# Optimization experiments

Hardware: AMD Instinct MI355X
Metric: run time of the kernel (lower is better)

The kernel has to match this reference:

```python
import jax, jax.numpy as jnp
import numpy as np

B, CQ, CKV, H, W = 8, 256, 512, 64, 64
HKV, WKV = 32, 32
DQK = CQ // 8  # 32


def setup_inputs() -> dict:
    key = jax.random.key(0)
    ks = jax.random.split(key, 9)
    s = 0.05
    return {
        "query": jax.random.normal(ks[0], (B, CQ, H, W), jnp.float32),
        "key_value": jax.random.normal(ks[1], (B, CKV, HKV, WKV), jnp.float32),
        "Wq": jax.random.normal(ks[2], (DQK, CQ), jnp.float32) * s,
        "bq": jax.random.normal(ks[3], (DQK,), jnp.float32) * s,
        "Wk": jax.random.normal(ks[4], (DQK, CKV), jnp.float32) * s,
        "bk": jax.random.normal(ks[5], (DQK,), jnp.float32) * s,
        "Wv": jax.random.normal(ks[6], (CQ, CKV), jnp.float32) * s,
        "bv": jax.random.normal(ks[7], (CQ,), jnp.float32) * s,
        "gamma": jax.random.normal(ks[8], (1,), jnp.float32) * 0.5,
    }


def reference(query, key_value, Wq, bq, Wk, bk, Wv, bv, gamma):
    b, cq, h, w = query.shape
    n = h * w
    # bilinear resize of key_value to query's spatial size (align_corners=False
    # half-pixel convention, matching torch F.interpolate and jax.image.resize)
    kv = jax.image.resize(key_value, (b, key_value.shape[1], h, w), method="bilinear")
    # 1x1 convs are channel contractions
    q = jnp.einsum("bchw,dc->bdhw", query, Wq) + bq[None, :, None, None]   # [B,DQK,H,W]
    k = jnp.einsum("bchw,dc->bdhw", kv, Wk) + bk[None, :, None, None]      # [B,DQK,H,W]
    v = jnp.einsum("bchw,dc->bdhw", kv, Wv) + bv[None, :, None, None]      # [B,CQ,H,W]
    qf = q.reshape(b, -1, n)   # [B,DQK,N]
    kf = k.reshape(b, -1, n)   # [B,DQK,N]
    vf = v.reshape(b, -1, n)   # [B,CQ,N]
    energy = jnp.einsum("bdn,bdm->bnm", qf, kf)        # [B,N,N]
    attention = jax.nn.softmax(energy, axis=-1)
    out = jnp.einsum("bnm,bcm->bcn", attention, vf)     # [B,CQ,N]
    out = out.reshape(b, cq, h, w)
    return gamma[0] * out + query
```

## Files before the change

### kernel.cpp

```cpp
#include <hip/hip_runtime.h>

#define B_ 8
#define CQ_ 256
#define CKV_ 512
#define N_ 4096
#define DQK_ 32

typedef __bf16 bf16;
typedef __bf16 bf16x4 __attribute__((ext_vector_type(4)));
typedef __bf16 bf16x8 __attribute__((ext_vector_type(8)));
typedef float f32x4 __attribute__((ext_vector_type(4)));

__global__ void k_convert_w(const float* __restrict__ Wq, const float* __restrict__ Wk,
                            const float* __restrict__ Wv,
                            bf16* __restrict__ wq, bf16* __restrict__ wk, bf16* __restrict__ wv) {
    int i = blockIdx.x * 256 + threadIdx.x;
    if (i < 8192) wq[i] = (bf16)Wq[i];
    else if (i < 24576) wk[i - 8192] = (bf16)Wk[i - 8192];
    else if (i < 155648) wv[i - 24576] = (bf16)Wv[i - 24576];
}

__global__ __launch_bounds__(256) void k_resize(const float* __restrict__ kv, bf16* __restrict__ kvr) {
    const int yo = blockIdx.x;
    const int b  = blockIdx.y;
    const int tid = threadIdx.x;
    __shared__ float r0[64][33];
    __shared__ float r1[64][33];
    int ty = yo >> 1;
    int y0, y1; float wy0, wy1;
    if ((yo & 1) == 0) { y0 = ty > 0 ? ty - 1 : 0; y1 = ty; wy0 = 0.25f; wy1 = 0.75f; }
    else               { y0 = ty; y1 = ty < 31 ? ty + 1 : 31; wy0 = 0.75f; wy1 = 0.25f; }
    const int u_loc = tid & 63;
    const int xo_base = tid >> 6;
    for (int uc = 0; uc < CKV_; uc += 64) {
        __syncthreads();
        for (int i = 0; i < 8; ++i) {
            int idx = tid + i * 256;
            int u = idx >> 5, x = idx & 31;
            const float* src = kv + ((size_t)b * CKV_ + uc + u) * 1024 + x;
            r0[u][x] = src[y0 * 32];
            r1[u][x] = src[y1 * 32];
        }
        __syncthreads();
        for (int i = 0; i < 16; ++i) {
            int xo = xo_base + i * 4;
            int tx = xo >> 1;
            int xa, xb; float wxa, wxb;
            if ((xo & 1) == 0) { xa = tx > 0 ? tx - 1 : 0; xb = tx; wxa = 0.25f; wxb = 0.75f; }
            else               { xa = tx; xb = tx < 31 ? tx + 1 : 31; wxa = 0.75f; wxb = 0.25f; }
            float v0 = wxa * r0[u_loc][xa] + wxb * r0[u_loc][xb];
            float v1 = wxa * r1[u_loc][xa] + wxb * r1[u_loc][xb];
            float val = wy0 * v0 + wy1 * v1;
            kvr[((size_t)b * N_ + yo * 64 + xo) * CKV_ + uc + u_loc] = (bf16)val;
        }
    }
}

__global__ __launch_bounds__(256) void k_proj_q_fused(const float* __restrict__ query,
                                                      const bf16* __restrict__ W,
                                                      const float* __restrict__ bias,
                                                      bf16* __restrict__ qTb) {
    __shared__ bf16 tile[64][264];
    const int n0 = blockIdx.x * 64;
    const int b  = blockIdx.y;
    const int tid = threadIdx.x;
    const int xi = tid & 15, c0 = tid >> 4;
    for (int pass = 0; pass < 16; ++pass) {
        int c = c0 + pass * 16;
        const float4 v = *(const float4*)(query + ((size_t)b * CQ_ + c) * N_ + n0 + xi * 4);
        tile[xi * 4 + 0][c] = (bf16)v.x;
        tile[xi * 4 + 1][c] = (bf16)v.y;
        tile[xi * 4 + 2][c] = (bf16)v.z;
        tile[xi * 4 + 3][c] = (bf16)v.w;
    }
    __syncthreads();
    const int w = tid >> 6, lane = tid & 63;
    const int l16 = lane & 15, quad = lane >> 4;
    const int ct = w & 1, nh = w >> 1;
    f32x4 acc[2];
    acc[0] = (f32x4){0.f, 0.f, 0.f, 0.f}; acc[1] = (f32x4){0.f, 0.f, 0.f, 0.f};
    const bf16* aptr = W + (ct * 16 + l16) * CQ_ + quad * 8;
#pragma unroll
    for (int ks = 0; ks < 8; ++ks) {
        bf16x8 af = *(const bf16x8*)(aptr + ks * 32);
        for (int j = 0; j < 2; ++j) {
            bf16x8 bfv = *(const bf16x8*)&tile[nh * 32 + j * 16 + l16][ks * 32 + quad * 8];
            acc[j] = __builtin_amdgcn_mfma_f32_16x16x32_bf16(af, bfv, acc[j], 0, 0, 0);
        }
    }
    const float LOG2E = 1.4426950408889634f;
    for (int j = 0; j < 2; ++j)
        for (int r = 0; r < 4; ++r) {
            int d = ct * 16 + quad * 4 + r;
            int n = n0 + nh * 32 + j * 16 + l16;
            qTb[((size_t)b * N_ + n) * DQK_ + d] = (bf16)((acc[j][r] + bias[d]) * LOG2E);
        }
}

__global__ __launch_bounds__(256) void k_proj_k(const bf16* __restrict__ W,
                                                const float* __restrict__ bias,
                                                const bf16* __restrict__ Bm,
                                                bf16* __restrict__ outT) {
    const int mb = blockIdx.x * 128;
    const int b  = blockIdx.y;
    const int tid = threadIdx.x;
    const int w = tid >> 6, lane = tid & 63;
    const int l16 = lane & 15, quad = lane >> 4;
    const int ct = w & 1;
    const int mhalf = (w >> 1) * 64;
    f32x4 acc[4];
    for (int j = 0; j < 4; ++j) acc[j] = (f32x4){0.f, 0.f, 0.f, 0.f};
    const bf16* aptr  = W + (ct * 16 + l16) * CKV_ + quad * 8;
    const bf16* bbase = Bm + ((size_t)b * N_ + mb + mhalf) * CKV_ + quad * 8;
#pragma unroll
    for (int ks = 0; ks < 16; ++ks) {
        bf16x8 af = *(const bf16x8*)(aptr + ks * 32);
        for (int j = 0; j < 4; ++j) {
            bf16x8 bfv = *(const bf16x8*)(bbase + (size_t)(j * 16 + l16) * CKV_ + ks * 32);
            acc[j] = __builtin_amdgcn_mfma_f32_16x16x32_bf16(af, bfv, acc[j], 0, 0, 0);
        }
    }
    for (int j = 0; j < 4; ++j)
        for (int r = 0; r < 4; ++r) {
            int d = ct * 16 + quad * 4 + r;
            int m = mb + mhalf + j * 16 + l16;
            outT[((size_t)b * N_ + m) * DQK_ + d] = (bf16)(acc[j][r] + bias[d]);
        }
}

__global__ __launch_bounds__(256) void k_proj_v(const bf16* __restrict__ W,
                                                const float* __restrict__ bias,
                                                const bf16* __restrict__ Bm,
                                                bf16* __restrict__ vout) {
    const int mb = blockIdx.x * 64;
    const int b  = blockIdx.y;
    const int tid = threadIdx.x;
    const int w = tid >> 6, lane = tid & 63;
    const int l16 = lane & 15, quad = lane >> 4;
    f32x4 acc[4][4];
    for (int i = 0; i < 4; ++i) for (int j = 0; j < 4; ++j) acc[i][j] = (f32x4){0.f, 0.f, 0.f, 0.f};
    const bf16* bbase = Bm + ((size_t)b * N_ + mb) * CKV_ + quad * 8;
#pragma unroll 4
    for (int ks = 0; ks < 16; ++ks) {
        bf16x8 bfv[4];
        for (int j = 0; j < 4; ++j)
            bfv[j] = *(const bf16x8*)(bbase + (size_t)(j * 16 + l16) * CKV_ + ks * 32);
        for (int i = 0; i < 4; ++i) {
            bf16x8 af = *(const bf16x8*)(W + (size_t)((w * 4 + i) * 16 + l16) * CKV_ + ks * 32 + quad * 8);
            for (int j = 0; j < 4; ++j)
                acc[i][j] = __builtin_amdgcn_mfma_f32_16x16x32_bf16(af, bfv[j], acc[i][j], 0, 0, 0);
        }
    }
    for (int i = 0; i < 4; ++i)
        for (int r = 0; r < 4; ++r) {
            int c = (w * 4 + i) * 16 + quad * 4 + r;
            float bvs = bias[c];
            for (int j = 0; j < 4; ++j) {
                int m = mb + j * 16 + l16;
                vout[((size_t)b * CQ_ + c) * N_ + m] = (bf16)(acc[i][j][r] + bvs);
            }
        }
}

__global__ __launch_bounds__(256, 2) void k_flash(const bf16* __restrict__ qT,
                                                  const bf16* __restrict__ kT,
                                                  const bf16* __restrict__ vv,
                                                  const float* __restrict__ query,
                                                  const float* __restrict__ gamma,
                                                  float* __restrict__ out) {
    __shared__ bf16 P[2][64][72];
    const int b  = blockIdx.x;
    const int n0 = blockIdx.y * 64;
    const int tid = threadIdx.x;
    const int w = tid >> 6, lane = tid & 63;
    const int l16 = lane & 15, quad = lane >> 4;
    const int swz = (l16 & 3) ^ ((l16 >> 3) << 1);

    bf16x8 qfrag = *(const bf16x8*)(qT + ((size_t)b * N_ + n0 + w * 16 + l16) * DQK_ + quad * 8);

    const bf16 one = (bf16)1.0f;
    const bf16x8 ones = {one, one, one, one, one, one, one, one};
    const f32x4 zed = {0.f, 0.f, 0.f, 0.f};

    f32x4 acc[4][4];
    for (int i = 0; i < 4; ++i) for (int j = 0; j < 4; ++j) acc[i][j] = zed;
    f32x4 accl[4];
    for (int j = 0; j < 4; ++j) accl[j] = zed;

    const bf16* kbase = kT + (size_t)b * N_ * DQK_;
    const bf16* vbase = vv + ((size_t)b * CQ_ + w * 64) * N_;

    for (int im = 0; im < 4; ++im) {
        bf16x8 kf = *(const bf16x8*)(kbase + (size_t)(im * 16 + l16) * DQK_ + quad * 8);
        f32x4 s = __builtin_amdgcn_mfma_f32_16x16x32_bf16(kf, qfrag, zed, 0, 0, 0);
        bf16x4 pk;
        for (int r = 0; r < 4; ++r) pk[r] = (bf16)__builtin_amdgcn_exp2f(s[r]);
        *(bf16x4*)&P[0][w * 16 + l16][((im ^ swz) << 4) + quad * 4] = pk;
    }

    for (int mt = 0; mt < 64; ++mt) {
        __syncthreads();
        const int m0 = mt * 64;
        bf16 (* __restrict__ Pb)[72] = P[mt & 1];
        bf16x8 pf[2][4];
        for (int ks = 0; ks < 2; ++ks)
            for (int j = 0; j < 4; ++j)
                pf[ks][j] = *(const bf16x8*)&Pb[j * 16 + l16]
                                [((((ks << 1) | (quad >> 1)) ^ swz) << 4) + ((quad & 1) << 3)];
        bf16x8 vf[2][4];
        for (int ks = 0; ks < 2; ++ks)
            for (int i = 0; i < 4; ++i)
                vf[ks][i] = *(const bf16x8*)(vbase + (size_t)(i * 16 + l16) * N_ + m0 + ks * 32 + quad * 8);
        if (mt < 63) {
            const int m1 = m0 + 64;
            bf16 (* __restrict__ Pn)[72] = P[(mt + 1) & 1];
            for (int im = 0; im < 4; ++im) {
                bf16x8 kf = *(const bf16x8*)(kbase + (size_t)(m1 + im * 16 + l16) * DQK_ + quad * 8);
                f32x4 s = __builtin_amdgcn_mfma_f32_16x16x32_bf16(kf, qfrag, zed, 0, 0, 0);
                bf16x4 pk;
                for (int r = 0; r < 4; ++r) pk[r] = (bf16)__builtin_amdgcn_exp2f(s[r]);
                *(bf16x4*)&Pn[w * 16 + l16][((im ^ swz) << 4) + quad * 4] = pk;
            }
        }
        for (int ks = 0; ks < 2; ++ks)
            for (int j = 0; j < 4; ++j) {
                accl[j] = __builtin_amdgcn_mfma_f32_16x16x32_bf16(ones, pf[ks][j], accl[j], 0, 0, 0);
                for (int i = 0; i < 4; ++i)
                    acc[i][j] = __builtin_amdgcn_mfma_f32_16x16x32_bf16(vf[ks][i], pf[ks][j], acc[i][j], 0, 0, 0);
            }
    }

    float linv[4];
    for (int j = 0; j < 4; ++j) linv[j] = 1.f / accl[j][0];
    const float g = gamma[0];
    for (int i = 0; i < 4; ++i)
        for (int r = 0; r < 4; ++r) {
            int c = w * 64 + i * 16 + quad * 4 + r;
            for (int j = 0; j < 4; ++j) {
                int n = n0 + j * 16 + l16;
                size_t idx = ((size_t)b * CQ_ + c) * N_ + n;
                out[idx] = g * acc[i][j][r] * linv[j] + query[idx];
            }
        }
}

extern "C" void kernel_launch(void* const* d_in, const int* in_sizes, int n_in,
                              void* d_out, int out_size, void* d_ws, size_t ws_size,
                              hipStream_t stream) {
    const float* query     = (const float*)d_in[0];
    const float* key_value = (const float*)d_in[1];
    const float* Wq = (const float*)d_in[2];
    const float* bq = (const float*)d_in[3];
    const float* Wk = (const float*)d_in[4];
    const float* bk = (const float*)d_in[5];
    const float* Wv = (const float*)d_in[6];
    const float* bv = (const float*)d_in[7];
    const float* gamma = (const float*)d_in[8];
    float* out = (float*)d_out;

    char* ws = (char*)d_ws;
    bf16* kvr  = (bf16*)(ws);
    bf16* vbuf = (bf16*)(ws + 33554432);
    bf16* qTb  = (bf16*)(ws + 50331648);
    bf16* kTb  = (bf16*)(ws + 52428800);
    bf16* wqb  = (bf16*)(ws + 54525952);
    bf16* wkb  = (bf16*)(ws + 54542336);
    bf16* wvb  = (bf16*)(ws + 54575104);

    k_convert_w<<<608, 256, 0, stream>>>(Wq, Wk, Wv, wqb, wkb, wvb);
    k_resize<<<dim3(64, 8), 256, 0, stream>>>(key_value, kvr);
    k_proj_q_fused<<<dim3(64, 8), 256, 0, stream>>>(query, wqb, bq, qTb);
    k_proj_k<<<dim3(32, 8), 256, 0, stream>>>(wkb, bk, kvr, kTb);
    k_proj_v<<<dim3(64, 8), 256, 0, stream>>>(wvb, bv, kvr, vbuf);
    k_flash<<<dim3(8, 64), 256, 0, stream>>>(qTb, kTb, vbuf, query, gamma, out);
}
```

Before: 355.2 us.

## Fuse KV resize with K/V projections and split flash attention over key halves

The bilinear resize now feeds an LDS tile that is consumed directly by MFMA K and V projections, so the 32 MB intermediate resized key/value buffer is never written to or read back from global memory. Flash attention is split into two key-range halves with a third grid dimension, and the launch bound asks for 4 blocks per CU. Each half writes unnormalized bf16 partial outputs and row sums, and a new combine kernel merges them with gamma and the residual. This adds a partial-output write/read pass and extra bf16 rounding in exchange for more parallelism. The workspace overlaps opart with the converted weights, which only works because the weights are consumed before flash runs.

Result: slower. 601.8 us (+69.4%).

```diff
diff --git a/kernel.cpp b/kernel.cpp
--- a/kernel.cpp
+++ b/kernel.cpp
@@ -20,21 +20,37 @@
     else if (i < 155648) wv[i - 24576] = (bf16)Wv[i - 24576];
 }
 
-__global__ __launch_bounds__(256) void k_resize(const float* __restrict__ kv, bf16* __restrict__ kvr) {
+__global__ __launch_bounds__(256) void k_resize_projkv(const float* __restrict__ kv,
+                                                       const bf16* __restrict__ Wk,
+                                                       const float* __restrict__ bk,
+                                                       const bf16* __restrict__ Wv,
+                                                       const float* __restrict__ bv,
+                                                       bf16* __restrict__ kTb,
+                                                       bf16* __restrict__ vbuf) {
+    __shared__ float r0[128][33];
+    __shared__ float r1[128][33];
+    __shared__ bf16 kvt[64][136];
     const int yo = blockIdx.x;
     const int b  = blockIdx.y;
     const int tid = threadIdx.x;
-    __shared__ float r0[64][33];
-    __shared__ float r1[64][33];
     int ty = yo >> 1;
     int y0, y1; float wy0, wy1;
     if ((yo & 1) == 0) { y0 = ty > 0 ? ty - 1 : 0; y1 = ty; wy0 = 0.25f; wy1 = 0.75f; }
     else               { y0 = ty; y1 = ty < 31 ? ty + 1 : 31; wy0 = 0.75f; wy1 = 0.25f; }
-    const int u_loc = tid & 63;
-    const int xo_base = tid >> 6;
-    for (int uc = 0; uc < CKV_; uc += 64) {
-        __syncthreads();
-        for (int i = 0; i < 8; ++i) {
+    const int w = tid >> 6, lane = tid & 63;
+    const int l16 = lane & 15, quad = lane >> 4;
+    const int ct = w & 1;
+    const int jp = w >> 1;
+    const int u_loc = tid & 127, xo2 = tid >> 7;
+
+    f32x4 acck[2];
+    acck[0] = (f32x4){0.f, 0.f, 0.f, 0.f}; acck[1] = (f32x4){0.f, 0.f, 0.f, 0.f};
+    f32x4 accv[4][4];
+    for (int i = 0; i < 4; ++i) for (int j = 0; j < 4; ++j) accv[i][j] = (f32x4){0.f, 0.f, 0.f, 0.f};
+
+    for (int uc = 0; uc < CKV_; uc += 128) {
+        __syncthreads();
+        for (int i = 0; i < 16; ++i) {
             int idx = tid + i * 256;
             int u = idx >> 5, x = idx & 31;
             const float* src = kv + ((size_t)b * CKV_ + uc + u) * 1024 + x;
@@ -42,18 +58,47 @@
             r1[u][x] = src[y1 * 32];
         }
         __syncthreads();
-        for (int i = 0; i < 16; ++i) {
-            int xo = xo_base + i * 4;
+        for (int i = 0; i < 32; ++i) {
+            int xo = xo2 + i * 2;
             int tx = xo >> 1;
             int xa, xb; float wxa, wxb;
             if ((xo & 1) == 0) { xa = tx > 0 ? tx - 1 : 0; xb = tx; wxa = 0.25f; wxb = 0.75f; }
             else               { xa = tx; xb = tx < 31 ? tx + 1 : 31; wxa = 0.75f; wxb = 0.25f; }
             float v0 = wxa * r0[u_loc][xa] + wxb * r0[u_loc][xb];
             float v1 = wxa * r1[u_loc][xa] + wxb * r1[u_loc][xb];
-            float val = wy0 * v0 + wy1 * v1;
-            kvr[((size_t)b * N_ + yo * 64 + xo) * CKV_ + uc + u_loc] = (bf16)val;
-        }
-    }
+            kvt[xo][u_loc] = (bf16)(wy0 * v0 + wy1 * v1);
+        }
+        __syncthreads();
+        for (int ks = 0; ks < 4; ++ks) {
+            bf16x8 bfv[4];
+            for (int j = 0; j < 4; ++j)
+                bfv[j] = *(const bf16x8*)&kvt[j * 16 + l16][ks * 32 + quad * 8];
+            bf16x8 afk = *(const bf16x8*)(Wk + (size_t)(ct * 16 + l16) * CKV_ + uc + ks * 32 + quad * 8);
+            acck[0] = __builtin_amdgcn_mfma_f32_16x16x32_bf16(afk, bfv[jp * 2 + 0], acck[0], 0, 0, 0);
+            acck[1] = __builtin_amdgcn_mfma_f32_16x16x32_bf16(afk, bfv[jp * 2 + 1], acck[1], 0, 0, 0);
+            for (int i = 0; i < 4; ++i) {
+                bf16x8 afv = *(const bf16x8*)(Wv + (size_t)((w * 4 + i) * 16 + l16) * CKV_ + uc + ks * 32 + quad * 8);
+                for (int j = 0; j < 4; ++j)
+                    accv[i][j] = __builtin_amdgcn_mfma_f32_16x16x32_bf16(afv, bfv[j], accv[i][j], 0, 0, 0);
+            }
+        }
+    }
+    const int m0 = yo * 64;
+    for (int jj = 0; jj < 2; ++jj)
+        for (int r = 0; r < 4; ++r) {
+            int d = ct * 16 + quad * 4 + r;
+            int m = m0 + (jp * 2 + jj) * 16 + l16;
+            kTb[((size_t)b * N_ + m) * DQK_ + d] = (bf16)(acck[jj][r] + bk[d]);
+        }
+    for (int i = 0; i < 4; ++i)
+        for (int r = 0; r < 4; ++r) {
+            int c = w * 64 + i * 16 + quad * 4 + r;
+            float bvs = bv[c];
+            for (int j = 0; j < 4; ++j) {
+                int m = m0 + j * 16 + l16;
+                vbuf[((size_t)b * CQ_ + c) * N_ + m] = (bf16)(accv[i][j][r] + bvs);
+            }
+        }
 }
 
 __global__ __launch_bounds__(256) void k_proj_q_fused(const float* __restrict__ query,
@@ -97,80 +142,16 @@
         }
 }
 
-__global__ __launch_bounds__(256) void k_proj_k(const bf16* __restrict__ W,
-                                                const float* __restrict__ bias,
-                                                const bf16* __restrict__ Bm,
-                                                bf16* __restrict__ outT) {
-    const int mb = blockIdx.x * 128;
-    const int b  = blockIdx.y;
-    const int tid = threadIdx.x;
-    const int w = tid >> 6, lane = tid & 63;
-    const int l16 = lane & 15, quad = lane >> 4;
-    const int ct = w & 1;
-    const int mhalf = (w >> 1) * 64;
-    f32x4 acc[4];
-    for (int j = 0; j < 4; ++j) acc[j] = (f32x4){0.f, 0.f, 0.f, 0.f};
-    const bf16* aptr  = W + (ct * 16 + l16) * CKV_ + quad * 8;
-    const bf16* bbase = Bm + ((size_t)b * N_ + mb + mhalf) * CKV_ + quad * 8;
-#pragma unroll
-    for (int ks = 0; ks < 16; ++ks) {
-        bf16x8 af = *(const bf16x8*)(aptr + ks * 32);
-        for (int j = 0; j < 4; ++j) {
-            bf16x8 bfv = *(const bf16x8*)(bbase + (size_t)(j * 16 + l16) * CKV_ + ks * 32);
-            acc[j] = __builtin_amdgcn_mfma_f32_16x16x32_bf16(af, bfv, acc[j], 0, 0, 0);
-        }
-    }
-    for (int j = 0; j < 4; ++j)
-        for (int r = 0; r < 4; ++r) {
-            int d = ct * 16 + quad * 4 + r;
-            int m = mb + mhalf + j * 16 + l16;
-            outT[((size_t)b * N_ + m) * DQK_ + d] = (bf16)(acc[j][r] + bias[d]);
-        }
-}
-
-__global__ __launch_bounds__(256) void k_proj_v(const bf16* __restrict__ W,
-                                                const float* __restrict__ bias,
-                                                const bf16* __restrict__ Bm,
-                                                bf16* __restrict__ vout) {
-    const int mb = blockIdx.x * 64;
-    const int b  = blockIdx.y;
-    const int tid = threadIdx.x;
-    const int w = tid >> 6, lane = tid & 63;
-    const int l16 = lane & 15, quad = lane >> 4;
-    f32x4 acc[4][4];
-    for (int i = 0; i < 4; ++i) for (int j = 0; j < 4; ++j) acc[i][j] = (f32x4){0.f, 0.f, 0.f, 0.f};
-    const bf16* bbase = Bm + ((size_t)b * N_ + mb) * CKV_ + quad * 8;
-#pragma unroll 4
-    for (int ks = 0; ks < 16; ++ks) {
-        bf16x8 bfv[4];
-        for (int j = 0; j < 4; ++j)
-            bfv[j] = *(const bf16x8*)(bbase + (size_t)(j * 16 + l16) * CKV_ + ks * 32);
-        for (int i = 0; i < 4; ++i) {
-            bf16x8 af = *(const bf16x8*)(W + (size_t)((w * 4 + i) * 16 + l16) * CKV_ + ks * 32 + quad * 8);
-            for (int j = 0; j < 4; ++j)
-                acc[i][j] = __builtin_amdgcn_mfma_f32_16x16x32_bf16(af, bfv[j], acc[i][j], 0, 0, 0);
-        }
-    }
-    for (int i = 0; i < 4; ++i)
-        for (int r = 0; r < 4; ++r) {
-            int c = (w * 4 + i) * 16 + quad * 4 + r;
-            float bvs = bias[c];
-            for (int j = 0; j < 4; ++j) {
-                int m = mb + j * 16 + l16;
-                vout[((size_t)b * CQ_ + c) * N_ + m] = (bf16)(acc[i][j][r] + bvs);
-            }
-        }
-}
-
-__global__ __launch_bounds__(256, 2) void k_flash(const bf16* __restrict__ qT,
+__global__ __launch_bounds__(256, 4) void k_flash(const bf16* __restrict__ qT,
                                                   const bf16* __restrict__ kT,
                                                   const bf16* __restrict__ vv,
-                                                  const float* __restrict__ query,
-                                                  const float* __restrict__ gamma,
-                                                  float* __restrict__ out) {
+                                                  bf16* __restrict__ opart,
+                                                  float* __restrict__ lpart) {
     __shared__ bf16 P[2][64][72];
     const int b  = blockIdx.x;
     const int n0 = blockIdx.y * 64;
+    const int z  = blockIdx.z;
+    const int mbase = z * (N_ / 2);
     const int tid = threadIdx.x;
     const int w = tid >> 6, lane = tid & 63;
     const int l16 = lane & 15, quad = lane >> 4;
@@ -191,16 +172,16 @@
     const bf16* vbase = vv + ((size_t)b * CQ_ + w * 64) * N_;
 
     for (int im = 0; im < 4; ++im) {
-        bf16x8 kf = *(const bf16x8*)(kbase + (size_t)(im * 16 + l16) * DQK_ + quad * 8);
+        bf16x8 kf = *(const bf16x8*)(kbase + (size_t)(mbase + im * 16 + l16) * DQK_ + quad * 8);
         f32x4 s = __builtin_amdgcn_mfma_f32_16x16x32_bf16(kf, qfrag, zed, 0, 0, 0);
         bf16x4 pk;
         for (int r = 0; r < 4; ++r) pk[r] = (bf16)__builtin_amdgcn_exp2f(s[r]);
         *(bf16x4*)&P[0][w * 16 + l16][((im ^ swz) << 4) + quad * 4] = pk;
     }
 
-    for (int mt = 0; mt < 64; ++mt) {
-        __syncthreads();
-        const int m0 = mt * 64;
+    for (int mt = 0; mt < 32; ++mt) {
+        __syncthreads();
+        const int m0 = mbase + mt * 64;
         bf16 (* __restrict__ Pb)[72] = P[mt & 1];
         bf16x8 pf[2][4];
         for (int ks = 0; ks < 2; ++ks)
@@ -211,7 +192,7 @@
         for (int ks = 0; ks < 2; ++ks)
             for (int i = 0; i < 4; ++i)
                 vf[ks][i] = *(const bf16x8*)(vbase + (size_t)(i * 16 + l16) * N_ + m0 + ks * 32 + quad * 8);
-        if (mt < 63) {
+        if (mt < 31) {
             const int m1 = m0 + 64;
             bf16 (* __restrict__ Pn)[72] = P[(mt + 1) & 1];
             for (int im = 0; im < 4; ++im) {
@@ -230,18 +211,40 @@
             }
     }
 
-    float linv[4];
-    for (int j = 0; j < 4; ++j) linv[j] = 1.f / accl[j][0];
-    const float g = gamma[0];
+    if (quad == 0)
+        for (int j = 0; j < 4; ++j)
+            lpart[((size_t)z * B_ + b) * N_ + n0 + j * 16 + l16] = accl[j][0];
+    bf16* ob = opart + (size_t)z * B_ * CQ_ * N_;
     for (int i = 0; i < 4; ++i)
         for (int r = 0; r < 4; ++r) {
             int c = w * 64 + i * 16 + quad * 4 + r;
             for (int j = 0; j < 4; ++j) {
                 int n = n0 + j * 16 + l16;
-                size_t idx = ((size_t)b * CQ_ + c) * N_ + n;
-                out[idx] = g * acc[i][j][r] * linv[j] + query[idx];
-            }
-        }
+                ob[((size_t)b * CQ_ + c) * N_ + n] = (bf16)acc[i][j][r];
+            }
+        }
+}
+
+__global__ __launch_bounds__(256) void k_combine(const bf16* __restrict__ opart,
+                                                 const float* __restrict__ lpart,
+                                                 const float* __restrict__ query,
+                                                 const float* __restrict__ gamma,
+                                                 float* __restrict__ out) {
+    const size_t i4 = ((size_t)blockIdx.x * 256 + threadIdx.x) * 4;
+    const int n = (int)(i4 & (N_ - 1));
+    const int b = (int)(i4 >> 20);
+    float4 l1 = *(const float4*)(lpart + (size_t)b * N_ + n);
+    float4 l2 = *(const float4*)(lpart + ((size_t)B_ + b) * N_ + n);
+    bf16x4 o1 = *(const bf16x4*)(opart + i4);
+    bf16x4 o2 = *(const bf16x4*)(opart + (size_t)B_ * CQ_ * N_ + i4);
+    float4 q = *(const float4*)(query + i4);
+    const float g = gamma[0];
+    float4 r;
+    r.x = g * ((float)o1[0] + (float)o2[0]) / (l1.x + l2.x) + q.x;
+    r.y = g * ((float)o1[1] + (float)o2[1]) / (l1.y + l2.y) + q.y;
+    r.z = g * ((float)o1[2] + (float)o2[2]) / (l1.z + l2.z) + q.z;
+    r.w = g * ((float)o1[3] + (float)o2[3]) / (l1.w + l2.w) + q.w;
+    *(float4*)(out + i4) = r;
 }
 
 extern "C" void kernel_launch(void* const* d_in, const int* in_sizes, int n_in,
@@ -259,18 +262,18 @@
     float* out = (float*)d_out;
 
     char* ws = (char*)d_ws;
-    bf16* kvr  = (bf16*)(ws);
-    bf16* vbuf = (bf16*)(ws + 33554432);
-    bf16* qTb  = (bf16*)(ws + 50331648);
-    bf16* kTb  = (bf16*)(ws + 52428800);
-    bf16* wqb  = (bf16*)(ws + 54525952);
-    bf16* wkb  = (bf16*)(ws + 54542336);
-    bf16* wvb  = (bf16*)(ws + 54575104);
+    bf16*  vbuf  = (bf16*)(ws);
+    bf16*  qTb   = (bf16*)(ws + 16777216);
+    bf16*  kTb   = (bf16*)(ws + 18874368);
+    float* lpart = (float*)(ws + 20971520);
+    bf16*  opart = (bf16*)(ws + 21233664);
+    bf16*  wqb   = (bf16*)(ws + 21233664);
+    bf16*  wkb   = (bf16*)(ws + 21250048);
+    bf16*  wvb   = (bf16*)(ws + 21282816);
 
     k_convert_w<<<608, 256, 0, stream>>>(Wq, Wk, Wv, wqb, wkb, wvb);
-    k_resize<<<dim3(64, 8), 256, 0, stream>>>(key_value, kvr);
+    k_resize_projkv<<<dim3(64, 8), 256, 0, stream>>>(key_value, wkb, bk, wvb, bv, kTb, vbuf);
     k_proj_q_fused<<<dim3(64, 8), 256, 0, stream>>>(query, wqb, bq, qTb);
-    k_proj_k<<<dim3(32, 8), 256, 0, stream>>>(wkb, bk, kvr, kTb);
-    k_proj_v<<<dim3(64, 8), 256, 0, stream>>>(wvb, bv, kvr, vbuf);
-    k_flash<<<dim3(8, 64), 256, 0, stream>>>(qTb, kTb, vbuf, query, gamma, out);
-}
+    k_flash<<<dim3(8, 64, 2), 256, 0, stream>>>(qTb, kTb, vbuf, opart, lpart);
+    k_combine<<<8192, 256, 0, stream>>>(opart, lpart, query, gamma, out);
+}
```
